# Kernel optimization log

Measured on AMD Instinct MI355X. Metric: run time of the kernel, lower is better.

Reference implementation:

```python
import jax, jax.numpy as jnp
import numpy as np

IN_DIM = 1024
OUT_DIM = 1024
NUM_HEADS = 16
DEPTH = IN_DIM // NUM_HEADS  # 64


def setup_inputs() -> dict:
    key = jax.random.key(0)
    ks = jax.random.split(key, 11)
    B, S = 8, 1024  # S must equal IN_DIM (reshape constraint in original module)
    s_in = 1.0 / np.sqrt(IN_DIM)
    return {
        "query": jax.random.normal(ks[0], (B, S, IN_DIM), jnp.float32),
        "key": jax.random.normal(ks[1], (B, S, IN_DIM), jnp.float32),
        "value": jax.random.normal(ks[2], (B, S, IN_DIM), jnp.float32),
        "Wq": jax.random.normal(ks[3], (IN_DIM, IN_DIM), jnp.float32) * s_in,
        "bq": jnp.zeros((IN_DIM,), jnp.float32),
        "Wk": jax.random.normal(ks[4], (IN_DIM, IN_DIM), jnp.float32) * s_in,
        "bk": jnp.zeros((IN_DIM,), jnp.float32),
        "Wv": jax.random.normal(ks[5], (IN_DIM, IN_DIM), jnp.float32) * s_in,
        "bv": jnp.zeros((IN_DIM,), jnp.float32),
        "Wo": jax.random.normal(ks[6], (OUT_DIM, IN_DIM), jnp.float32) * s_in,
        "bo": jnp.zeros((OUT_DIM,), jnp.float32),
    }


def reference(query, key, value, Wq, bq, Wk, bk, Wv, bv, Wo, bo):
    B, S, D = query.shape
    H, P = NUM_HEADS, DEPTH

    def split_heads(x):
        # (B,S,D) -> (B,S,H,P) -> transpose last two dims -> (B,S,P,H)
        return x.reshape(B, S, H, P).swapaxes(-1, -2)

    Q = split_heads(query @ Wq.T + bq)   # (B,S,P,H)
    K = split_heads(key @ Wk.T + bk)     # (B,S,P,H)
    V = split_heads(value @ Wv.T + bv)   # (B,S,P,H)

    scale = jnp.sqrt(jnp.float32(P))
    # scores over the depth axis, per (batch, token): (B,S,P,P)
    scores = jnp.einsum('bsph,bsqh->bspq', Q, K) / scale
    # original uses softmax over dim=0 (the batch axis) - reproduce faithfully
    attn = jax.nn.softmax(scores, axis=0)
    out = jnp.einsum('bspq,bsqh->bsph', attn, V)   # (B,S,P,H)
    # transpose(-1,-2) -> (B,S,H,P), reshape to (B,S,S) (requires H*P == S)
    out = out.swapaxes(-1, -2).reshape(B, S, S)
    out = out @ Wo.T + bo                           # (B,S,OUT_DIM)
    return jax.nn.sigmoid(out)
```

## Files before the change

### kernel.cpp

```cpp
#include <hip/hip_runtime.h>


using short8   = __attribute__((ext_vector_type(8))) short;
using floatx4  = __attribute__((ext_vector_type(4))) float;
using floatx16 = __attribute__((ext_vector_type(16))) float;

__device__ __forceinline__ float bf2f(unsigned short u) {
    return __uint_as_float(((unsigned)u) << 16);
}
__device__ __forceinline__ unsigned short f2bf(float f) {
    unsigned u = __float_as_uint(f);
    u += 0x7fffu + ((u >> 16) & 1u);
    return (unsigned short)(u >> 16);
}
__device__ __forceinline__ unsigned pack_trunc(float f0, float f1) {
    return __builtin_amdgcn_perm(__float_as_uint(f1), __float_as_uint(f0), 0x07060302u);
}
__device__ __forceinline__ void async_ld16(const void* g, void* l) {
    __builtin_amdgcn_global_load_lds(
        (const __attribute__((address_space(1))) unsigned int*)g,
        (__attribute__((address_space(3))) unsigned int*)l, 16, 0, 0);
}
__device__ __forceinline__ short8 lds_read_b128(unsigned addr) {
    short8 r;
    asm volatile("ds_read_b128 %0, %1" : "=v"(r) : "v"(addr));
    return r;
}

__device__ __forceinline__ void conv8(const float* src, unsigned short* d, size_t i) {
    float4 a = *(const float4*)(src + i);
    float4 b = *(const float4*)(src + i + 4);
    uint4 o;
    o.x = ((unsigned)f2bf(a.y) << 16) | f2bf(a.x);
    o.y = ((unsigned)f2bf(a.w) << 16) | f2bf(a.z);
    o.z = ((unsigned)f2bf(b.y) << 16) | f2bf(b.x);
    o.w = ((unsigned)f2bf(b.w) << 16) | f2bf(b.z);
    *(uint4*)(d + i) = o;
}

__global__ __launch_bounds__(256) void convert_weights(
    const float* __restrict__ w0, const float* __restrict__ w1,
    const float* __restrict__ w2, const float* __restrict__ w3,
    unsigned short* __restrict__ dst)
{
    const float* srcs[4] = {w0, w1, w2, w3};
    conv8(srcs[blockIdx.y], dst + (size_t)blockIdx.y * (1024u * 1024u),
          ((size_t)blockIdx.x * 256 + threadIdx.x) * 8);
}

__global__ __launch_bounds__(256) void convert_acts(
    const float* __restrict__ a0, const float* __restrict__ a1,
    const float* __restrict__ a2, unsigned short* __restrict__ dst)
{
    const float* srcs[3] = {a0, a1, a2};
    conv8(srcs[blockIdx.y], dst + (size_t)blockIdx.y * ((size_t)8192 * 1024),
          ((size_t)blockIdx.x * 256 + threadIdx.x) * 8);
}

template<bool AF32, bool SIG>
__global__ __launch_bounds__(256) void gemm128(
    const void* __restrict__ A0, const void* __restrict__ A1, const void* __restrict__ A2,
    const unsigned short* __restrict__ W0, const unsigned short* __restrict__ W1,
    const unsigned short* __restrict__ W2,
    const float* __restrict__ b0, const float* __restrict__ b1, const float* __restrict__ b2,
    void* __restrict__ C0, void* __restrict__ C1, void* __restrict__ C2)
{
    const int z = blockIdx.z;
    const void* Ap = (z == 0) ? A0 : (z == 1) ? A1 : A2;
    const unsigned short* W = (z == 0) ? W0 : (z == 1) ? W1 : W2;
    const float* bias = (z == 0) ? b0 : (z == 1) ? b1 : b2;
    void* Cp = (z == 0) ? C0 : (z == 1) ? C1 : C2;

    constexpr int Kd = 1024, Nd = 1024;
    const int t = threadIdx.x;
    const int w = t >> 6, lane = t & 63;
    const int l15 = lane & 15, quad = lane >> 4;
    const int blockM = blockIdx.x * 128;
    const int blockN = blockIdx.y * 128;
    const int wy = w >> 1, wx = w & 1;

    __shared__ unsigned short Bs[128 * 32];
    constexpr int ABYTES = AF32 ? (128 * 32 * 4) : (128 * 32 * 2);
    __shared__ __align__(16) unsigned char AsRaw[ABYTES];
    float* AsF = (float*)AsRaw;
    unsigned short* AsB = (unsigned short*)AsRaw;

    const int br  = lane >> 2;
    const int bg  = (lane & 3) ^ (br & 3);
    const unsigned short* Bsrc0 = W + (size_t)(blockN + w * 32 + br) * Kd + bg * 8;
    const unsigned short* Bsrc1 = Bsrc0 + (size_t)16 * Kd;
    unsigned short* Bdst0 = &Bs[(w * 2 + 0) * 512];
    unsigned short* Bdst1 = &Bs[(w * 2 + 1) * 512];

    const int ar = lane >> 3;
    const int ag = (lane & 7) ^ (ar & 7);
    const float* AsrcF[4];
    float* AdstF[4];
    const unsigned short* AsrcB0 = nullptr; const unsigned short* AsrcB1 = nullptr;
    unsigned short* AdstB0 = nullptr; unsigned short* AdstB1 = nullptr;
    if (AF32) {
        #pragma unroll
        for (int j = 0; j < 4; ++j) {
            AsrcF[j] = (const float*)Ap + (size_t)(blockM + w * 32 + j * 8 + ar) * Kd + ag * 4;
            AdstF[j] = AsF + (w * 4 + j) * 256;
        }
    } else {
        AsrcB0 = (const unsigned short*)Ap + (size_t)(blockM + w * 32 + br) * Kd + bg * 8;
        AsrcB1 = AsrcB0 + (size_t)16 * Kd;
        AdstB0 = &AsB[(w * 2 + 0) * 512];
        AdstB1 = &AsB[(w * 2 + 1) * 512];
    }

    floatx4 acc[4][4] = {};

    for (int k0 = 0; k0 < Kd; k0 += 32) {
        if (AF32) {
            #pragma unroll
            for (int j = 0; j < 4; ++j) async_ld16(AsrcF[j] + k0, AdstF[j]);
        } else {
            async_ld16(AsrcB0 + k0, AdstB0);
            async_ld16(AsrcB1 + k0, AdstB1);
        }
        async_ld16(Bsrc0 + k0, Bdst0);
        async_ld16(Bsrc1 + k0, Bdst1);
        __syncthreads();

        short8 af[4], bfr[4];
        #pragma unroll
        for (int mt = 0; mt < 4; ++mt) {
            const int row = wy * 64 + mt * 16 + l15;
            if (AF32) {
                const int r7 = l15 & 7;
                const float* ap = AsF + row * 32;
                float4 lo = *(const float4*)(ap + (((quad * 2 + 0) ^ r7) * 4));
                float4 hi = *(const float4*)(ap + (((quad * 2 + 1) ^ r7) * 4));
                union { unsigned u[4]; short8 s; } cv;
                cv.u[0] = pack_trunc(lo.x, lo.y);
                cv.u[1] = pack_trunc(lo.z, lo.w);
                cv.u[2] = pack_trunc(hi.x, hi.y);
                cv.u[3] = pack_trunc(hi.z, hi.w);
                af[mt] = cv.s;
            } else {
                af[mt] = *(const short8*)&AsB[row * 32 + (quad ^ (l15 & 3)) * 8];
            }
        }
        #pragma unroll
        for (int nt = 0; nt < 4; ++nt) {
            const int row = wx * 64 + nt * 16 + l15;
            bfr[nt] = *(const short8*)&Bs[row * 32 + (quad ^ (l15 & 3)) * 8];
        }
        #pragma unroll
        for (int mt = 0; mt < 4; ++mt)
            #pragma unroll
            for (int nt = 0; nt < 4; ++nt)
                acc[mt][nt] = __builtin_amdgcn_mfma_f32_16x16x32_bf16(af[mt], bfr[nt], acc[mt][nt], 0, 0, 0);
        __syncthreads();
    }

    #pragma unroll
    for (int nt = 0; nt < 4; ++nt) {
        const int col = blockN + wx * 64 + nt * 16 + l15;
        const float bv = bias[col];
        #pragma unroll
        for (int mt = 0; mt < 4; ++mt) {
            const int row = blockM + wy * 64 + mt * 16 + quad * 4;
            #pragma unroll
            for (int r = 0; r < 4; ++r) {
                float v = acc[mt][nt][r] + bv;
                if (SIG) {
                    v = 1.0f / (1.0f + __expf(-v));
                    ((float*)Cp)[(size_t)(row + r) * Nd + col] = v;
                } else {
                    ((unsigned short*)Cp)[(size_t)(row + r) * Nd + col] = f2bf(v);
                }
            }
        }
    }
}

#define VM8 do { asm volatile("s_waitcnt vmcnt(8)" ::: "memory"); \
                 __builtin_amdgcn_sched_barrier(0); } while (0)
#define VM4 do { asm volatile("s_waitcnt vmcnt(4)" ::: "memory"); \
                 __builtin_amdgcn_sched_barrier(0); } while (0)
#define VM0 do { asm volatile("s_waitcnt vmcnt(0)" ::: "memory"); \
                 __builtin_amdgcn_sched_barrier(0); } while (0)
#define LGKM0 do { asm volatile("s_waitcnt lgkmcnt(0)" ::: "memory"); \
                   __builtin_amdgcn_sched_barrier(0); } while (0)
#define BARRIER __builtin_amdgcn_s_barrier()

#define STAGE_T(s, k0) do { \
    async_ld16(srcA[0] + (k0), &lds[s][0][dA0]); \
    async_ld16(srcA[1] + (k0), &lds[s][0][dA1]); \
    async_ld16(srcB[0] + (k0), &lds[s][1][dA0]); \
    async_ld16(srcB[1] + (k0), &lds[s][1][dA1]); \
} while (0)

#define PHASE_T(s, STG, VMW) do { \
    const unsigned bA_ = (unsigned)(size_t)&lds[s][0][0]; \
    const unsigned bB_ = (unsigned)(size_t)&lds[s][1][0]; \
    short8 afr[4][2], bfr2[2][2]; \
    _Pragma("unroll") \
    for (int mf = 0; mf < 4; ++mf) \
      _Pragma("unroll") \
      for (int ks = 0; ks < 2; ++ks) \
        afr[mf][ks] = lds_read_b128(bA_ + (unsigned)aoffB[mf][ks]); \
    _Pragma("unroll") \
    for (int nf = 0; nf < 2; ++nf) \
      _Pragma("unroll") \
      for (int ks = 0; ks < 2; ++ks) \
        bfr2[nf][ks] = lds_read_b128(bB_ + (unsigned)boffB[nf][ks]); \
    STG; \
    VMW; \
    BARRIER; \
    LGKM0; \
    __builtin_amdgcn_s_setprio(1); \
    _Pragma("unroll") \
    for (int ks = 0; ks < 2; ++ks) \
      _Pragma("unroll") \
      for (int mf = 0; mf < 4; ++mf) \
        _Pragma("unroll") \
        for (int nf = 0; nf < 2; ++nf) \
          acc[mf][nf] = __builtin_amdgcn_mfma_f32_32x32x16_bf16( \
              afr[mf][ks], bfr2[nf][ks], acc[mf][nf], 0, 0, 0); \
    __builtin_amdgcn_s_setprio(0); \
    BARRIER; \
} while (0)

template<bool SIG>
__global__ __launch_bounds__(512, 2) void gemm256(
    const unsigned short* __restrict__ A0, const unsigned short* __restrict__ A1,
    const unsigned short* __restrict__ A2,
    const unsigned short* __restrict__ W0, const unsigned short* __restrict__ W1,
    const unsigned short* __restrict__ W2,
    const float* __restrict__ b0, const float* __restrict__ b1, const float* __restrict__ b2,
    void* __restrict__ C0, void* __restrict__ C1, void* __restrict__ C2)
{
    const int z = blockIdx.z;
    const unsigned short* A = (z == 0) ? A0 : (z == 1) ? A1 : A2;
    const unsigned short* W = (z == 0) ? W0 : (z == 1) ? W1 : W2;
    const float* bias = (z == 0) ? b0 : (z == 1) ? b1 : b2;
    void* Cp = (z == 0) ? C0 : (z == 1) ? C1 : C2;

    constexpr int Kd = 1024;
    const int t = threadIdx.x;
    const int w = t >> 6, l = t & 63;
    const int wy = w >> 2, wx = w & 3;
    const int l31 = l & 31, h5 = l >> 5;
    const int blockM = blockIdx.x * 256;
    const int blockN = blockIdx.y * 256;

    __shared__ __align__(16) unsigned short lds[4][2][8192];

    const unsigned short* srcA[2];
    const unsigned short* srcB[2];
    #pragma unroll
    for (int i = 0; i < 2; ++i) {
        const int q  = i * 512 + w * 64 + l;
        const int L  = q >> 3;
        const int Gr = (q & 7) ^ (L & 7);
        const int r  = L * 2 + (Gr >> 2);
        const int g  = Gr & 3;
        srcA[i] = A + (size_t)(blockM + r) * Kd + g * 8;
        srcB[i] = W + (size_t)(blockN + r) * Kd + g * 8;
    }
    const int dA0 = (0 * 512 + w * 64) * 8;
    const int dA1 = (1 * 512 + w * 64) * 8;

    const int Lh  = l31 >> 1;
    const int la7 = Lh & 7;
    const int e4  = (l & 1) * 4;
    int aoffB[4][2], boffB[2][2];
    #pragma unroll
    for (int mf = 0; mf < 4; ++mf)
        #pragma unroll
        for (int ks = 0; ks < 2; ++ks)
            aoffB[mf][ks] = ((wy * 64 + mf * 16 + Lh) * 64 + ((e4 + ks * 2 + h5) ^ la7) * 8) * 2;
    #pragma unroll
    for (int nf = 0; nf < 2; ++nf)
        #pragma unroll
        for (int ks = 0; ks < 2; ++ks)
            boffB[nf][ks] = ((wx * 32 + nf * 16 + Lh) * 64 + ((e4 + ks * 2 + h5) ^ la7) * 8) * 2;

    floatx16 acc[4][2] = {};

    STAGE_T(0, 0); STAGE_T(1, 32); STAGE_T(2, 64);
    VM8;
    BARRIER;

    int k0 = 96;
    #pragma unroll 1
    for (int tt = 0; tt < 28; tt += 4) {
        PHASE_T(0, STAGE_T(3, k0), VM8); k0 += 32;
        PHASE_T(1, STAGE_T(0, k0), VM8); k0 += 32;
        PHASE_T(2, STAGE_T(1, k0), VM8); k0 += 32;
        PHASE_T(3, STAGE_T(2, k0), VM8); k0 += 32;
    }
    PHASE_T(0, STAGE_T(3, k0), VM8);
    PHASE_T(1, (void)0, VM4);
    PHASE_T(2, (void)0, VM0);
    PHASE_T(3, (void)0, (void)0);

    const int colBase = blockN + wx * 64 + l31;
    const float bv0 = bias[colBase];
    const float bv1 = bias[colBase + 32];
    #pragma unroll
    for (int mf = 0; mf < 4; ++mf) {
        const int row0 = blockM + wy * 128 + mf * 32 + h5 * 4;
        #pragma unroll
        for (int nf = 0; nf < 2; ++nf) {
            const float bb = nf ? bv1 : bv0;
            const int col = colBase + nf * 32;
            #pragma unroll
            for (int rg = 0; rg < 16; ++rg) {
                const int row = row0 + (rg & 3) + 8 * (rg >> 2);
                float v = acc[mf][nf][rg] + bb;
                if (SIG) {
                    v = 1.0f / (1.0f + __expf(-v));
                    ((float*)Cp)[(size_t)row * 1024 + col] = v;
                } else {
                    ((unsigned short*)Cp)[(size_t)row * 1024 + col] = f2bf(v);
                }
            }
        }
    }
}

__global__ __launch_bounds__(512) void attn_mfma(
    const unsigned short* __restrict__ Q,
    const unsigned short* __restrict__ Kt,
    const unsigned short* __restrict__ Vt,
    unsigned short* __restrict__ O2)
{
    constexpr int VOFF = 0;
    constexpr int UOFF = 9216;
    constexpr int QOFF = UOFF + 8192;
    __shared__ __align__(16) unsigned short lds[UOFF + 18432];

    const int s  = blockIdx.x;
    const int ph = blockIdx.y;
    const int t  = threadIdx.x;
    const int w  = t >> 6;
    const int l  = t & 63;
    const int l15 = l & 15, l31 = l & 31, half = l >> 5, quad = l >> 4;

    const size_t gb = ((size_t)w * 1024 + s) * 1024;

    {
        const unsigned* vg = (const unsigned*)(Vt + gb);
        unsigned* vd = (unsigned*)lds;
        #pragma unroll
        for (int it = 0; it < 8; ++it) {
            const int h = it * 2 + half;
            vd[w * 576 + h * 36 + l31] = vg[h * 32 + l31];
        }
        const unsigned short* kg = Kt + gb;
        unsigned* kd = (unsigned*)(lds + UOFF);
        #pragma unroll
        for (int h2 = 0; h2 < 8; ++h2) {
            unsigned klo = kg[(2 * h2) * 64 + l];
            unsigned khi = kg[(2 * h2 + 1) * 64 + l];
            kd[w * 512 + l * 8 + h2] = klo | (khi << 16);
        }
        const unsigned short* qg = Q + gb + ph * 32;
        unsigned* qd = (unsigned*)(lds + QOFF);
        #pragma unroll
        for (int it = 0; it < 4; ++it) {
            const int h = it * 4 + half * 2;
            unsigned qlo = qg[h * 64 + l31];
            unsigned qhi = qg[(h + 1) * 64 + l31];
            qd[w * 256 + l31 * 8 + it * 2 + half] = qlo | (qhi << 16);
        }
    }
    __syncthreads();

    floatx16 sc[2];
    {
        short8 qf = *(const short8*)&lds[QOFF + w * 512 + l31 * 16 + half * 8];
        short8 kf0 = *(const short8*)&lds[UOFF + w * 1024 + l31 * 16 + half * 8];
        short8 kf1 = *(const short8*)&lds[UOFF + w * 1024 + (32 + l31) * 16 + half * 8];
        floatx16 z = {};
        sc[0] = __builtin_amdgcn_mfma_f32_32x32x16_bf16(kf0, qf, z, 0, 0, 0);
        sc[1] = __builtin_amdgcn_mfma_f32_32x32x16_bf16(kf1, qf, z, 0, 0, 0);
    }
    __syncthreads();

    {
        unsigned short* sx = lds + UOFF + w * 2304 + l31 * 72;
        #pragma unroll
        for (int nt = 0; nt < 2; ++nt) {
            #pragma unroll
            for (int rg = 0; rg < 4; ++rg) {
                float e0 = __expf(sc[nt][4 * rg + 0] * 0.125f);
                float e1 = __expf(sc[nt][4 * rg + 1] * 0.125f);
                float e2 = __expf(sc[nt][4 * rg + 2] * 0.125f);
                float e3 = __expf(sc[nt][4 * rg + 3] * 0.125f);
                uint2 pk = { pack_trunc(e0, e1), pack_trunc(e2, e3) };
                const int q0 = nt * 32 + rg * 8 + half * 4;
                *(uint2*)&sx[q0] = pk;
            }
        }
    }
    __syncthreads();

    {
        const int p  = t & 31;
        const int q0 = (t >> 5) * 4;
        unsigned short* base = lds + UOFF + p * 72 + q0;
        float fv[8][4];
        float den0 = 0.f, den1 = 0.f, den2 = 0.f, den3 = 0.f;
        #pragma unroll
        for (int b = 0; b < 8; ++b) {
            uint2 v = *(const uint2*)&base[b * 2304];
            fv[b][0] = bf2f((unsigned short)(v.x & 0xffff));
            fv[b][1] = bf2f((unsigned short)(v.x >> 16));
            fv[b][2] = bf2f((unsigned short)(v.y & 0xffff));
            fv[b][3] = bf2f((unsigned short)(v.y >> 16));
            den0 += fv[b][0]; den1 += fv[b][1]; den2 += fv[b][2]; den3 += fv[b][3];
        }
        const float r0 = __builtin_amdgcn_rcpf(den0);
        const float r1 = __builtin_amdgcn_rcpf(den1);
        const float r2 = __builtin_amdgcn_rcpf(den2);
        const float r3 = __builtin_amdgcn_rcpf(den3);
        #pragma unroll
        for (int b = 0; b < 8; ++b) {
            uint2 pk = { pack_trunc(fv[b][0] * r0, fv[b][1] * r1),
                         pack_trunc(fv[b][2] * r2, fv[b][3] * r3) };
            *(uint2*)&base[b * 2304] = pk;
        }
    }
    __syncthreads();

    floatx4 o[2] = {};
    #pragma unroll
    for (int qc = 0; qc < 2; ++qc) {
        short8 vf = *(const short8*)&lds[VOFF + w * 1152 + l15 * 72 + qc * 32 + quad * 8];
        #pragma unroll
        for (int mt = 0; mt < 2; ++mt) {
            short8 wf = *(const short8*)&lds[UOFF + w * 2304 + (mt * 16 + l15) * 72 + qc * 32 + quad * 8];
            o[mt] = __builtin_amdgcn_mfma_f32_16x16x32_bf16(wf, vf, o[mt], 0, 0, 0);
        }
    }
    {
        unsigned short* ol = lds + UOFF + w * 2304 + l15 * 36;
        #pragma unroll
        for (int mt = 0; mt < 2; ++mt) {
            uint2 pk = { pack_trunc(o[mt][0], o[mt][1]), pack_trunc(o[mt][2], o[mt][3]) };
            *(uint2*)&ol[mt * 16 + quad * 4] = pk;
        }
    }
    __syncthreads();

    {
        unsigned* outdw = (unsigned*)O2;
        const unsigned* ol = (const unsigned*)(lds + UOFF + w * 2304);
        const size_t gdw = ((size_t)w * 1024 + s) * 512 + ph * 16;
        #pragma unroll
        for (int i = 0; i < 4; ++i) {
            const int d = i * 64 + l;
            const int h = d >> 4, pq = d & 15;
            outdw[gdw + h * 32 + pq] = ol[h * 18 + pq];
        }
    }
}

extern "C" void kernel_launch(void* const* d_in, const int* in_sizes, int n_in,
                              void* d_out, int out_size, void* d_ws, size_t ws_size,
                              hipStream_t stream) {
    const float* query = (const float*)d_in[0];
    const float* key_  = (const float*)d_in[1];
    const float* value = (const float*)d_in[2];
    const float* Wq = (const float*)d_in[3];
    const float* bq = (const float*)d_in[4];
    const float* Wk = (const float*)d_in[5];
    const float* bk = (const float*)d_in[6];
    const float* Wv = (const float*)d_in[7];
    const float* bv = (const float*)d_in[8];
    const float* Wo = (const float*)d_in[9];
    const float* bo = (const float*)d_in[10];

    const size_t WN = (size_t)1024 * 1024;
    const size_t MN = (size_t)8192 * 1024;

    unsigned short* Wbf = (unsigned short*)d_ws;
    unsigned short* Wq_bf = Wbf;
    unsigned short* Wk_bf = Wbf + WN;
    unsigned short* Wv_bf = Wbf + 2 * WN;
    unsigned short* Wo_bf = Wbf + 3 * WN;

    convert_weights<<<dim3(512, 4), dim3(256), 0, stream>>>(Wq, Wk, Wv, Wo, Wbf);

    const bool big = ws_size >= (4 * WN + 6 * MN) * sizeof(unsigned short);

    unsigned short* Qb; unsigned short* Kb; unsigned short* Vb;
    if (big) {
        unsigned short* abf = Wbf + 4 * WN;
        Qb = abf + 3 * MN; Kb = Qb + MN; Vb = Kb + MN;
        convert_acts<<<dim3(4096, 3), dim3(256), 0, stream>>>(query, key_, value, abf);
        gemm256<false><<<dim3(32, 4, 3), dim3(512), 0, stream>>>(
            abf, abf + MN, abf + 2 * MN, Wq_bf, Wk_bf, Wv_bf, bq, bk, bv, Qb, Kb, Vb);
    } else {
        Qb = Wbf + 4 * WN; Kb = Qb + MN; Vb = Kb + MN;
        gemm128<true, false><<<dim3(64, 8, 3), dim3(256), 0, stream>>>(
            query, key_, value, Wq_bf, Wk_bf, Wv_bf, bq, bk, bv, Qb, Kb, Vb);
    }

    unsigned short* O2 = Qb;
    attn_mfma<<<dim3(1024, 2), dim3(512), 0, stream>>>(Qb, Kb, Vb, O2);

    gemm128<false, true><<<dim3(64, 8, 1), dim3(256), 0, stream>>>(
        O2, O2, O2, Wo_bf, Wo_bf, Wo_bf, bo, bo, bo, d_out, d_out, d_out);
}
```

Measured before the change: 287.6 us.

## Restructure bf16 GEMM into eight-phase pipelined schedule and use it for output projection

Replaces the 4-stage GEMM main loop with an 8-phase schedule over 128KB of LDS. Each K half-tile is split into two M halves, and A and B async loads are staged separately and interleaved with the MFMA work to overlap loads with compute more finely. The output projection now uses this 256x256-tile kernel with a fused sigmoid instead of the 128-tile kernel. The fp32 path also switches from truncating to round-to-nearest bf16 packing, which costs extra ALU work. Using 128KB of LDS per block may limit occupancy despite the launch-bounds hint of 2 blocks.

```diff
diff --git a/kernel.cpp b/kernel.cpp
--- a/kernel.cpp
+++ b/kernel.cpp
@@ -16,6 +16,9 @@
 __device__ __forceinline__ unsigned pack_trunc(float f0, float f1) {
     return __builtin_amdgcn_perm(__float_as_uint(f1), __float_as_uint(f0), 0x07060302u);
 }
+__device__ __forceinline__ unsigned pack_rne(float f0, float f1) {
+    return (unsigned)f2bf(f0) | ((unsigned)f2bf(f1) << 16);
+}
 __device__ __forceinline__ void async_ld16(const void* g, void* l) {
     __builtin_amdgcn_global_load_lds(
         (const __attribute__((address_space(1))) unsigned int*)g,
@@ -31,10 +34,10 @@
     float4 a = *(const float4*)(src + i);
     float4 b = *(const float4*)(src + i + 4);
     uint4 o;
-    o.x = ((unsigned)f2bf(a.y) << 16) | f2bf(a.x);
-    o.y = ((unsigned)f2bf(a.w) << 16) | f2bf(a.z);
-    o.z = ((unsigned)f2bf(b.y) << 16) | f2bf(b.x);
-    o.w = ((unsigned)f2bf(b.w) << 16) | f2bf(b.z);
+    o.x = pack_rne(a.x, a.y);
+    o.y = pack_rne(a.z, a.w);
+    o.z = pack_rne(b.x, b.y);
+    o.w = pack_rne(b.z, b.w);
     *(uint4*)(d + i) = o;
 }
 
@@ -135,10 +138,10 @@
                 float4 lo = *(const float4*)(ap + (((quad * 2 + 0) ^ r7) * 4));
                 float4 hi = *(const float4*)(ap + (((quad * 2 + 1) ^ r7) * 4));
                 union { unsigned u[4]; short8 s; } cv;
-                cv.u[0] = pack_trunc(lo.x, lo.y);
-                cv.u[1] = pack_trunc(lo.z, lo.w);
-                cv.u[2] = pack_trunc(hi.x, hi.y);
-                cv.u[3] = pack_trunc(hi.z, hi.w);
+                cv.u[0] = pack_rne(lo.x, lo.y);
+                cv.u[1] = pack_rne(lo.z, lo.w);
+                cv.u[2] = pack_rne(hi.x, hi.y);
+                cv.u[3] = pack_rne(hi.z, hi.w);
                 af[mt] = cv.s;
             } else {
                 af[mt] = *(const short8*)&AsB[row * 32 + (quad ^ (l15 & 3)) * 8];
@@ -178,56 +181,50 @@
     }
 }
 
-#define VM8 do { asm volatile("s_waitcnt vmcnt(8)" ::: "memory"); \
-                 __builtin_amdgcn_sched_barrier(0); } while (0)
-#define VM4 do { asm volatile("s_waitcnt vmcnt(4)" ::: "memory"); \
-                 __builtin_amdgcn_sched_barrier(0); } while (0)
-#define VM0 do { asm volatile("s_waitcnt vmcnt(0)" ::: "memory"); \
-                 __builtin_amdgcn_sched_barrier(0); } while (0)
+#define VMW10 do { asm volatile("s_waitcnt vmcnt(10)" ::: "memory"); } while (0)
+#define VMW8  do { asm volatile("s_waitcnt vmcnt(8)"  ::: "memory"); } while (0)
+#define VMW4  do { asm volatile("s_waitcnt vmcnt(4)"  ::: "memory"); } while (0)
+#define VMW0  do { asm volatile("s_waitcnt vmcnt(0)"  ::: "memory"); } while (0)
 #define LGKM0 do { asm volatile("s_waitcnt lgkmcnt(0)" ::: "memory"); \
                    __builtin_amdgcn_sched_barrier(0); } while (0)
 #define BARRIER __builtin_amdgcn_s_barrier()
 
-#define STAGE_T(s, k0) do { \
-    async_ld16(srcA[0] + (k0), &lds[s][0][dA0]); \
-    async_ld16(srcA[1] + (k0), &lds[s][0][dA1]); \
-    async_ld16(srcB[0] + (k0), &lds[s][1][dA0]); \
-    async_ld16(srcB[1] + (k0), &lds[s][1][dA1]); \
+#define STG_A(BUF, KH, KE) do { \
+    async_ld16(pA[0] + (KE), &lds[(BUF)*32768 + (KH)*16384 + dstW]); \
+    async_ld16(pA[1] + (KE), &lds[(BUF)*32768 + (KH)*16384 + 8192 + dstW]); \
 } while (0)
-
-#define PHASE_T(s, STG, VMW) do { \
-    const unsigned bA_ = (unsigned)(size_t)&lds[s][0][0]; \
-    const unsigned bB_ = (unsigned)(size_t)&lds[s][1][0]; \
-    short8 afr[4][2], bfr2[2][2]; \
+#define STG_B(BUF, KH, KE) do { \
+    async_ld16(pB[0] + (KE), &lds[65536 + (BUF)*32768 + (KH)*16384 + dstW]); \
+    async_ld16(pB[1] + (KE), &lds[65536 + (BUF)*32768 + (KH)*16384 + 8192 + dstW]); \
+} while (0)
+
+#define RD_A(BUF, KH, MH) do { \
+    const unsigned rbA_ = (BUF)*32768u + (KH)*16384u; \
+    aF[0][0] = lds_read_b128(aRd[(MH)*2+0][0] + rbA_); \
+    aF[0][1] = lds_read_b128(aRd[(MH)*2+0][1] + rbA_); \
+    aF[1][0] = lds_read_b128(aRd[(MH)*2+1][0] + rbA_); \
+    aF[1][1] = lds_read_b128(aRd[(MH)*2+1][1] + rbA_); \
+} while (0)
+#define RD_B(BUF, KH) do { \
+    const unsigned rbB_ = (BUF)*32768u + (KH)*16384u; \
+    bF[0][0] = lds_read_b128(bRd[0][0] + rbB_); \
+    bF[0][1] = lds_read_b128(bRd[0][1] + rbB_); \
+    bF[1][0] = lds_read_b128(bRd[1][0] + rbB_); \
+    bF[1][1] = lds_read_b128(bRd[1][1] + rbB_); \
+} while (0)
+#define MM(MH) do { \
     _Pragma("unroll") \
-    for (int mf = 0; mf < 4; ++mf) \
+    for (int ks_ = 0; ks_ < 2; ++ks_) \
       _Pragma("unroll") \
-      for (int ks = 0; ks < 2; ++ks) \
-        afr[mf][ks] = lds_read_b128(bA_ + (unsigned)aoffB[mf][ks]); \
-    _Pragma("unroll") \
-    for (int nf = 0; nf < 2; ++nf) \
-      _Pragma("unroll") \
-      for (int ks = 0; ks < 2; ++ks) \
-        bfr2[nf][ks] = lds_read_b128(bB_ + (unsigned)boffB[nf][ks]); \
-    STG; \
-    VMW; \
-    BARRIER; \
-    LGKM0; \
-    __builtin_amdgcn_s_setprio(1); \
-    _Pragma("unroll") \
-    for (int ks = 0; ks < 2; ++ks) \
-      _Pragma("unroll") \
-      for (int mf = 0; mf < 4; ++mf) \
+      for (int af_ = 0; af_ < 2; ++af_) \
         _Pragma("unroll") \
-        for (int nf = 0; nf < 2; ++nf) \
-          acc[mf][nf] = __builtin_amdgcn_mfma_f32_32x32x16_bf16( \
-              afr[mf][ks], bfr2[nf][ks], acc[mf][nf], 0, 0, 0); \
-    __builtin_amdgcn_s_setprio(0); \
-    BARRIER; \
+        for (int nf_ = 0; nf_ < 2; ++nf_) \
+          acc[(MH)*2+af_][nf_] = __builtin_amdgcn_mfma_f32_32x32x16_bf16( \
+              aF[af_][ks_], bF[nf_][ks_], acc[(MH)*2+af_][nf_], 0, 0, 0); \
 } while (0)
 
 template<bool SIG>
-__global__ __launch_bounds__(512, 2) void gemm256(
+__global__ __launch_bounds__(512, 2) void gemm8p(
     const unsigned short* __restrict__ A0, const unsigned short* __restrict__ A1,
     const unsigned short* __restrict__ A2,
     const unsigned short* __restrict__ W0, const unsigned short* __restrict__ W1,
@@ -241,7 +238,6 @@
     const float* bias = (z == 0) ? b0 : (z == 1) ? b1 : b2;
     void* Cp = (z == 0) ? C0 : (z == 1) ? C1 : C2;
 
-    constexpr int Kd = 1024;
     const int t = threadIdx.x;
     const int w = t >> 6, l = t & 63;
     const int wy = w >> 2, wx = w & 3;
@@ -249,56 +245,66 @@
     const int blockM = blockIdx.x * 256;
     const int blockN = blockIdx.y * 256;
 
-    __shared__ __align__(16) unsigned short lds[4][2][8192];
-
-    const unsigned short* srcA[2];
-    const unsigned short* srcB[2];
+    __shared__ __align__(16) unsigned char lds[131072];
+
+    const unsigned ldsBase = (unsigned)(size_t)&lds[0];
+    const int swz = (l31 >> 1) & 3;
+    unsigned aRd[4][2], bRd[2][2];
+    #pragma unroll
+    for (int mf = 0; mf < 4; ++mf)
+        #pragma unroll
+        for (int ks = 0; ks < 2; ++ks)
+            aRd[mf][ks] = ldsBase + (unsigned)((wy * 128 + mf * 32 + l31) * 64)
+                          + (unsigned)((((ks * 2 + h5) ^ swz)) * 16);
+    #pragma unroll
+    for (int nf = 0; nf < 2; ++nf)
+        #pragma unroll
+        for (int ks = 0; ks < 2; ++ks)
+            bRd[nf][ks] = ldsBase + 65536u + (unsigned)((wx * 64 + nf * 32 + l31) * 64)
+                          + (unsigned)((((ks * 2 + h5) ^ swz)) * 16);
+
+    const unsigned short* pA[2];
+    const unsigned short* pB[2];
     #pragma unroll
     for (int i = 0; i < 2; ++i) {
-        const int q  = i * 512 + w * 64 + l;
-        const int L  = q >> 3;
-        const int Gr = (q & 7) ^ (L & 7);
-        const int r  = L * 2 + (Gr >> 2);
-        const int g  = Gr & 3;
-        srcA[i] = A + (size_t)(blockM + r) * Kd + g * 8;
-        srcB[i] = W + (size_t)(blockN + r) * Kd + g * 8;
-    }
-    const int dA0 = (0 * 512 + w * 64) * 8;
-    const int dA1 = (1 * 512 + w * 64) * 8;
-
-    const int Lh  = l31 >> 1;
-    const int la7 = Lh & 7;
-    const int e4  = (l & 1) * 4;
-    int aoffB[4][2], boffB[2][2];
-    #pragma unroll
-    for (int mf = 0; mf < 4; ++mf)
-        #pragma unroll
-        for (int ks = 0; ks < 2; ++ks)
-            aoffB[mf][ks] = ((wy * 64 + mf * 16 + Lh) * 64 + ((e4 + ks * 2 + h5) ^ la7) * 8) * 2;
-    #pragma unroll
-    for (int nf = 0; nf < 2; ++nf)
-        #pragma unroll
-        for (int ks = 0; ks < 2; ++ks)
-            boffB[nf][ks] = ((wx * 32 + nf * 16 + Lh) * 64 + ((e4 + ks * 2 + h5) ^ la7) * 8) * 2;
-
+        const int q = i * 512 + t;
+        const int r = q >> 2;
+        const int g = (q & 3) ^ ((r >> 1) & 3);
+        pA[i] = A + (size_t)(blockM + r) * 1024 + g * 8;
+        pB[i] = W + (size_t)(blockN + r) * 1024 + g * 8;
+    }
+    const int dstW = w * 1024;
+
+    short8 aF[2][2], bF[2][2];
     floatx16 acc[4][2] = {};
 
-    STAGE_T(0, 0); STAGE_T(1, 32); STAGE_T(2, 64);
-    VM8;
+    STG_B(0, 0, 0);  STG_A(0, 0, 0);
+    STG_B(0, 1, 32); STG_A(0, 1, 32);
+    STG_B(1, 0, 64); STG_A(1, 0, 64);
+    STG_B(1, 1, 96);
+    VMW10;
     BARRIER;
 
-    int k0 = 96;
     #pragma unroll 1
-    for (int tt = 0; tt < 28; tt += 4) {
-        PHASE_T(0, STAGE_T(3, k0), VM8); k0 += 32;
-        PHASE_T(1, STAGE_T(0, k0), VM8); k0 += 32;
-        PHASE_T(2, STAGE_T(1, k0), VM8); k0 += 32;
-        PHASE_T(3, STAGE_T(2, k0), VM8); k0 += 32;
-    }
-    PHASE_T(0, STAGE_T(3, k0), VM8);
-    PHASE_T(1, (void)0, VM4);
-    PHASE_T(2, (void)0, VM0);
-    PHASE_T(3, (void)0, (void)0);
+    for (int i = 0; i < 7; ++i) {
+        const int kb = i * 128;
+        RD_A(0,0,0); RD_B(0,0); STG_A(1,1, kb +  96); LGKM0; MM(0);        BARRIER;
+        RD_A(0,0,1);            STG_B(0,0, kb + 128); LGKM0; MM(1); VMW10; BARRIER;
+        RD_A(0,1,0); RD_B(0,1); STG_A(0,0, kb + 128); LGKM0; MM(0);        BARRIER;
+        RD_A(0,1,1);            STG_B(0,1, kb + 160); LGKM0; MM(1); VMW10; BARRIER;
+        RD_A(1,0,0); RD_B(1,0); STG_A(0,1, kb + 160); LGKM0; MM(0);        BARRIER;
+        RD_A(1,0,1);            STG_B(1,0, kb + 192); LGKM0; MM(1); VMW10; BARRIER;
+        RD_A(1,1,0); RD_B(1,1); STG_A(1,0, kb + 192); LGKM0; MM(0);        BARRIER;
+        RD_A(1,1,1);            STG_B(1,1, kb + 224); LGKM0; MM(1); VMW10; BARRIER;
+    }
+    RD_A(0,0,0); RD_B(0,0); STG_A(1,1, 992); LGKM0; MM(0);        BARRIER;
+    RD_A(0,0,1);                             LGKM0; MM(1); VMW8;  BARRIER;
+    RD_A(0,1,0); RD_B(0,1);                  LGKM0; MM(0);        BARRIER;
+    RD_A(0,1,1);                             LGKM0; MM(1); VMW4;  BARRIER;
+    RD_A(1,0,0); RD_B(1,0);                  LGKM0; MM(0);        BARRIER;
+    RD_A(1,0,1);                             LGKM0; MM(1); VMW0;  BARRIER;
+    RD_A(1,1,0); RD_B(1,1);                  LGKM0; MM(0);        BARRIER;
+    RD_A(1,1,1);                             LGKM0; MM(1);
 
     const int colBase = blockN + wx * 64 + l31;
     const float bv0 = bias[colBase];
@@ -496,7 +502,7 @@
         unsigned short* abf = Wbf + 4 * WN;
         Qb = abf + 3 * MN; Kb = Qb + MN; Vb = Kb + MN;
         convert_acts<<<dim3(4096, 3), dim3(256), 0, stream>>>(query, key_, value, abf);
-        gemm256<false><<<dim3(32, 4, 3), dim3(512), 0, stream>>>(
+        gemm8p<false><<<dim3(32, 4, 3), dim3(512), 0, stream>>>(
             abf, abf + MN, abf + 2 * MN, Wq_bf, Wk_bf, Wv_bf, bq, bk, bv, Qb, Kb, Vb);
     } else {
         Qb = Wbf + 4 * WN; Kb = Qb + MN; Vb = Kb + MN;
@@ -507,6 +513,6 @@
     unsigned short* O2 = Qb;
     attn_mfma<<<dim3(1024, 2), dim3(512), 0, stream>>>(Qb, Kb, Vb, O2);
 
-    gemm128<false, true><<<dim3(64, 8, 1), dim3(256), 0, stream>>>(
+    gemm8p<true><<<dim3(32, 4, 1), dim3(512), 0, stream>>>(
         O2, O2, O2, Wo_bf, Wo_bf, Wo_bf, bo, bo, bo, d_out, d_out, d_out);
 }
```

Result: faster. 281.6 us (-2.1%).
